# Performance work log

Measured on AMD Instinct MI355X. Metric: run time of the kernel, lower is better.

The kernel has to match this reference:

```python
import jax, jax.numpy as jnp
import numpy as np
import math

INPUT_SIZE = 4096
PTS_PER_EPOCH = 100


def _grid_bounds(input_size):
    # Replicates get_grid(): n_row = n_col = ceil(sqrt(input_size)),
    # each cell is the central half of its grid square (gap = size/4 on each side).
    n = math.ceil(math.sqrt(input_size))
    size = 1.0 / n
    gap = size / 4.0
    i = jnp.arange(input_size)
    gy = i // n  # row index (uses n_row == n_col)
    gx = i % n
    x_low = gx.astype(jnp.float32) * size + gap
    y_low = gy.astype(jnp.float32) * size + gap
    x_high = x_low + 2.0 * gap
    y_high = y_low + 2.0 * gap
    return x_low, x_high, y_low, y_high


def setup_inputs() -> dict:
    key = jax.random.key(0)
    k1, k2, k3 = jax.random.split(key, 3)
    batch = 8192
    n_fibers = 64
    total_pts = 10000  # 100 * max_epoch
    inp = jax.random.normal(k1, (batch, INPUT_SIZE), dtype=jnp.float32)
    fibers_x = jax.random.uniform(k2, (n_fibers, total_pts), dtype=jnp.float32)
    fibers_y = jax.random.uniform(k3, (n_fibers, total_pts), dtype=jnp.float32)
    return {"input": inp, "fibers_x": fibers_x, "fibers_y": fibers_y, "current_epoch": 7}


def reference(input, fibers_x, fibers_y, current_epoch):
    t = current_epoch * PTS_PER_EPOCH
    # points of all fibers for this epoch, flattened: (P,) with P = n_fibers*100
    px = fibers_x[:, t:t + PTS_PER_EPOCH].reshape(-1)
    py = fibers_y[:, t:t + PTS_PER_EPOCH].reshape(-1)
    x_low, x_high, y_low, y_high = _grid_bounds(INPUT_SIZE)
    # broadcast point-in-rectangle test: (P, 1) vs (N,) -> (P, N)
    in_cell = ((x_low[None, :] <= px[:, None]) & (px[:, None] <= x_high[None, :]) &
               (y_low[None, :] <= py[:, None]) & (py[:, None] <= y_high[None, :]))
    touching = jnp.any(in_cell, axis=0)  # (N,)
    mask = jnp.where(touching, 0.0, 1.0).astype(input.dtype)
    return input * mask[None, :]
```

## Files before the change

### kernel.cpp

```cpp
#include <hip/hip_runtime.h>


#define N_COLS 4096
#define PTS_PER_EPOCH 100
#define N_GRID 64
#define TOTAL_PTS 10000
#define N_FIBERS 64

__global__ void build_mask_kernel(const float* __restrict__ fx,
                                  const float* __restrict__ fy,
                                  const int* __restrict__ epoch_p,
                                  float* __restrict__ mask) {
    const int tid = threadIdx.x;
    for (int i = tid; i < N_COLS; i += blockDim.x) mask[i] = 1.0f;
    __syncthreads();

    const int t = epoch_p[0] * PTS_PER_EPOCH;
    const int P = N_FIBERS * PTS_PER_EPOCH;
    for (int p = tid; p < P; p += blockDim.x) {
        const int f = p / PTS_PER_EPOCH;
        const int j = p - f * PTS_PER_EPOCH;
        const float px = fx[f * TOTAL_PTS + t + j];
        const float py = fy[f * TOTAL_PTS + t + j];
        const float ux = px * 64.0f;
        const float uy = py * 64.0f;
        const float gxf = floorf(ux);
        const float gyf = floorf(uy);
        const float frx = ux - gxf;
        const float fry = uy - gyf;
        if (frx >= 0.25f && frx <= 0.75f && fry >= 0.25f && fry <= 0.75f) {
            const int gx = (int)gxf;
            const int gy = (int)gyf;
            if (gx >= 0 && gx < N_GRID && gy >= 0 && gy < N_GRID) {
                mask[gy * N_GRID + gx] = 0.0f;
            }
        }
    }
}

__global__ void apply_mask_kernel(const float4* __restrict__ in4,
                                  const float4* __restrict__ mask4,
                                  float4* __restrict__ out4,
                                  int n4) {
    const int i = blockIdx.x * blockDim.x + threadIdx.x;
    if (i >= n4) return;
    const float4 a = in4[i];
    const float4 m = mask4[i & (N_COLS / 4 - 1)];
    float4 r;
    r.x = a.x * m.x;
    r.y = a.y * m.y;
    r.z = a.z * m.z;
    r.w = a.w * m.w;
    out4[i] = r;
}

extern "C" void kernel_launch(void* const* d_in, const int* in_sizes, int n_in,
                              void* d_out, int out_size, void* d_ws, size_t ws_size,
                              hipStream_t stream) {
    const float* inp   = (const float*)d_in[0];
    const float* fx    = (const float*)d_in[1];
    const float* fy    = (const float*)d_in[2];
    const int*   epoch = (const int*)d_in[3];
    float* out  = (float*)d_out;
    float* mask = (float*)d_ws;

    build_mask_kernel<<<1, 1024, 0, stream>>>(fx, fy, epoch, mask);

    const int n4 = out_size / 4;
    const int block = 256;
    const int grid = (n4 + block - 1) / block;
    apply_mask_kernel<<<grid, block, 0, stream>>>(
        (const float4*)inp, (const float4*)mask, (float4*)out, n4);
}
```

Before: 236.1 us.

## Fuse mask build into apply kernel with per-block shared-memory mask

Merges the single-block mask-building kernel and the elementwise apply kernel into one launch. Each of 2048 blocks rebuilds the full 4096-entry mask in shared memory from 6400 fiber points, loading them as float4. It then grid-strides over the input with a fixed per-thread mask float4. This removes one launch and the serial single-block stage, but repeats the mask construction in every block. The float4 loads assume the epoch offset is 4-aligned.

```diff
diff --git a/kernel.cpp b/kernel.cpp
--- a/kernel.cpp
+++ b/kernel.cpp
@@ -6,52 +6,62 @@
 #define N_GRID 64
 #define TOTAL_PTS 10000
 #define N_FIBERS 64
+#define BLOCK 256
+#define GRID_BLOCKS 2048
 
-__global__ void build_mask_kernel(const float* __restrict__ fx,
-                                  const float* __restrict__ fy,
-                                  const int* __restrict__ epoch_p,
-                                  float* __restrict__ mask) {
+__global__ __launch_bounds__(BLOCK) void fused_fbm_dropout(
+    const float* __restrict__ fx,
+    const float* __restrict__ fy,
+    const int* __restrict__ epoch_p,
+    const float4* __restrict__ in4,
+    float4* __restrict__ out4,
+    int n4) {
+    __shared__ float mask[N_COLS];
     const int tid = threadIdx.x;
-    for (int i = tid; i < N_COLS; i += blockDim.x) mask[i] = 1.0f;
+
+    for (int i = tid; i < N_COLS; i += BLOCK) mask[i] = 1.0f;
     __syncthreads();
 
     const int t = epoch_p[0] * PTS_PER_EPOCH;
-    const int P = N_FIBERS * PTS_PER_EPOCH;
-    for (int p = tid; p < P; p += blockDim.x) {
-        const int f = p / PTS_PER_EPOCH;
-        const int j = p - f * PTS_PER_EPOCH;
-        const float px = fx[f * TOTAL_PTS + t + j];
-        const float py = fy[f * TOTAL_PTS + t + j];
-        const float ux = px * 64.0f;
-        const float uy = py * 64.0f;
-        const float gxf = floorf(ux);
-        const float gyf = floorf(uy);
-        const float frx = ux - gxf;
-        const float fry = uy - gyf;
-        if (frx >= 0.25f && frx <= 0.75f && fry >= 0.25f && fry <= 0.75f) {
-            const int gx = (int)gxf;
-            const int gy = (int)gyf;
-            if (gx >= 0 && gx < N_GRID && gy >= 0 && gy < N_GRID) {
-                mask[gy * N_GRID + gx] = 0.0f;
+    for (int g = tid; g < (N_FIBERS * PTS_PER_EPOCH) / 4; g += BLOCK) {
+        const int f  = g / 25;
+        const int j4 = g - f * 25;
+        const int base4 = (f * TOTAL_PTS + t) / 4 + j4;
+        const float4 px4 = ((const float4*)fx)[base4];
+        const float4 py4 = ((const float4*)fy)[base4];
+        const float pxs[4] = {px4.x, px4.y, px4.z, px4.w};
+        const float pys[4] = {py4.x, py4.y, py4.z, py4.w};
+#pragma unroll
+        for (int k = 0; k < 4; ++k) {
+            const float ux = pxs[k] * 64.0f;
+            const float uy = pys[k] * 64.0f;
+            const float gxf = floorf(ux);
+            const float gyf = floorf(uy);
+            const float frx = ux - gxf;
+            const float fry = uy - gyf;
+            if (frx >= 0.25f && frx <= 0.75f && fry >= 0.25f && fry <= 0.75f) {
+                const int gx = (int)gxf;
+                const int gy = (int)gyf;
+                if (gx >= 0 && gx < N_GRID && gy >= 0 && gy < N_GRID) {
+                    mask[gy * N_GRID + gx] = 0.0f;
+                }
             }
         }
     }
-}
+    __syncthreads();
 
-__global__ void apply_mask_kernel(const float4* __restrict__ in4,
-                                  const float4* __restrict__ mask4,
-                                  float4* __restrict__ out4,
-                                  int n4) {
-    const int i = blockIdx.x * blockDim.x + threadIdx.x;
-    if (i >= n4) return;
-    const float4 a = in4[i];
-    const float4 m = mask4[i & (N_COLS / 4 - 1)];
-    float4 r;
-    r.x = a.x * m.x;
-    r.y = a.y * m.y;
-    r.z = a.z * m.z;
-    r.w = a.w * m.w;
-    out4[i] = r;
+    const int i0 = blockIdx.x * BLOCK + tid;
+    const float4 m = ((const float4*)mask)[i0 & (N_COLS / 4 - 1)];
+    const int stride = GRID_BLOCKS * BLOCK;
+    for (int i = i0; i < n4; i += stride) {
+        const float4 a = in4[i];
+        float4 r;
+        r.x = a.x * m.x;
+        r.y = a.y * m.y;
+        r.z = a.z * m.z;
+        r.w = a.w * m.w;
+        out4[i] = r;
+    }
 }
 
 extern "C" void kernel_launch(void* const* d_in, const int* in_sizes, int n_in,
@@ -61,14 +71,8 @@
     const float* fx    = (const float*)d_in[1];
     const float* fy    = (const float*)d_in[2];
     const int*   epoch = (const int*)d_in[3];
-    float* out  = (float*)d_out;
-    float* mask = (float*)d_ws;
-
-    build_mask_kernel<<<1, 1024, 0, stream>>>(fx, fy, epoch, mask);
 
     const int n4 = out_size / 4;
-    const int block = 256;
-    const int grid = (n4 + block - 1) / block;
-    apply_mask_kernel<<<grid, block, 0, stream>>>(
-        (const float4*)inp, (const float4*)mask, (float4*)out, n4);
+    fused_fbm_dropout<<<GRID_BLOCKS, BLOCK, 0, stream>>>(
+        fx, fy, epoch, (const float4*)inp, (float4*)d_out, n4);
 }
```

Measured after the change: 246.9 us. +4.6%, slower.
